# Optimization experiments

Hardware: AMD Instinct MI355X
Metric: run time of the kernel (lower is better)

Reference implementation:

```python
import jax, jax.numpy as jnp
import numpy as np

N, E, F = 32768, 524288, 16          # nodes, edges, num_filters
S_IN, V_IN = 64, 32                  # input irreps: 64x0e + 32x1o  (dim 64 + 96 = 160)
NRBF = 32                            # radial basis size of f_ij
LN2 = float(np.log(2.0))

def ssp(x):
    # shifted softplus, the standard SchNet activation
    return jax.nn.softplus(x) - LN2

def setup_inputs() -> dict:
    key = jax.random.key(0)
    ks = jax.random.split(key, 16)
    x = jax.random.normal(ks[0], (N, S_IN + 3 * V_IN), jnp.float32)
    idx_i = jax.random.randint(ks[1], (E,), 0, N)
    idx_j = jax.random.randint(ks[2], (E,), 0, N)
    f_ij = jax.random.normal(ks[3], (E, NRBF), jnp.float32)
    rcut_ij = jax.random.uniform(ks[4], (E,), jnp.float32)
    Yr_ij = jax.random.normal(ks[5], (E, 4), jnp.float32)  # 1x0e + 1x1o
    # equivariant Linear 1: (64x0e+32x1o) -> num_filters*(1x0e+1x1o) = 16x0e+16x1o
    W1_0e = jax.random.normal(ks[6], (S_IN, F), jnp.float32)
    W1_1o = jax.random.normal(ks[7], (V_IN, F), jnp.float32)
    # filter MLP: NRBF -> F -> num_irreps(6*F)
    mW1 = jax.random.normal(ks[8], (NRBF, F), jnp.float32) / np.sqrt(NRBF)
    mb1 = jnp.zeros((F,), jnp.float32)
    mW2 = jax.random.normal(ks[9], (F, 6 * F), jnp.float32) / np.sqrt(F)
    mb2 = jnp.zeros((6 * F,), jnp.float32)
    # equivariant Linear 2: (2Fx0e+2Fx1o+Fx1e+Fx2e) -> input irreps (1e/2e paths drop)
    W2_0e = jax.random.normal(ks[10], (2 * F, S_IN), jnp.float32)
    W2_1o = jax.random.normal(ks[11], (2 * F, V_IN), jnp.float32)
    # equivariant Linear 3: input irreps -> input irreps
    W3_0e = jax.random.normal(ks[12], (S_IN, S_IN), jnp.float32)
    W3_1o = jax.random.normal(ks[13], (V_IN, V_IN), jnp.float32)
    return dict(x=x, f_ij=f_ij, rcut_ij=rcut_ij, Yr_ij=Yr_ij,
                W1_0e=W1_0e, W1_1o=W1_1o, mW1=mW1, mb1=mb1, mW2=mW2, mb2=mb2,
                W2_0e=W2_0e, W2_1o=W2_1o, W3_0e=W3_0e, W3_1o=W3_1o,
                idx_i=idx_i, idx_j=idx_j)

def reference(x, f_ij, rcut_ij, Yr_ij, W1_0e, W1_1o, mW1, mb1, mW2, mb2,
              W2_0e, W2_1o, W3_0e, W3_1o, idx_i, idx_j):
    n = x.shape[0]
    s = x[:, :S_IN]                                  # [N, 64]  0e channels
    v = x[:, S_IN:].reshape(n, V_IN, 3)              # [N, 32, 3] 1o channels
    # Linear 1 (per-irrep channel mixing, e3nn fan-in normalization)
    s1 = (s @ W1_0e) / np.sqrt(S_IN)                 # [N, F]
    v1 = jnp.einsum('ncd,cf->nfd', v, W1_1o) / np.sqrt(V_IN)  # [N, F, 3]
    # gather neighbor features (x_j = x[idx_j], mul_to_axis -> per-filter irreps)
    sj = s1[idx_j]                                   # [E, F]
    vj = v1[idx_j]                                   # [E, F, 3]
    y0 = Yr_ij[:, 0]                                 # [E]
    y1 = Yr_ij[:, 1:4]                               # [E, 3]
    # tensor product (0e+1o) x (0e+1o) -> 2x0e + 2x1o + 1x1e + 1x2e, per filter
    o0a = sj * y0[:, None]                                            # 0e: 0e x 0e
    o0b = jnp.einsum('efd,ed->ef', vj, y1) / np.sqrt(3.0)             # 0e: 1o.1o
    o1a = sj[:, :, None] * y1[:, None, :]                             # 1o: 0e x 1o
    o1b = vj * y0[:, None, None]                                      # 1o: 1o x 0e
    o1e = jnp.cross(vj, y1[:, None, :]) / np.sqrt(2.0)                # 1e: 1o ^ 1o
    ux, uy, uz = vj[..., 0], vj[..., 1], vj[..., 2]
    wx, wy, wz = y1[:, None, 0], y1[:, None, 1], y1[:, None, 2]
    o2 = jnp.stack([(ux * wy + uy * wx) / np.sqrt(2.0),
                    (uy * wz + uz * wy) / np.sqrt(2.0),
                    (2.0 * uz * wz - ux * wx - uy * wy) / np.sqrt(6.0),
                    (ux * wz + uz * wx) / np.sqrt(2.0),
                    (ux * wx - uy * wy) / np.sqrt(2.0)], axis=-1)      # 2e [E, F, 5]
    # filter MLP on radial features, gated by cutoff; one scalar per irrep
    W = ssp(f_ij @ mW1 + mb1) @ mW2 + mb2            # [E, 6F]
    W = W * rcut_ij[:, None]
    w0a, w0b, w1a, w1b, w1e, w2 = (W[:, k * F:(k + 1) * F] for k in range(6))
    seg = lambda z: jax.ops.segment_sum(z, idx_i, num_segments=N)
    # modulate + scatter-sum into center atoms
    n0a = seg(o0a * w0a); n0b = seg(o0b * w0b)                          # [N, F]
    n1a = seg(o1a * w1a[:, :, None]); n1b = seg(o1b * w1b[:, :, None])  # [N, F, 3]
    n1e = seg(o1e * w1e[:, :, None])                                    # [N, F, 3] (dropped by Linear 2)
    n2 = seg(o2 * w2[:, :, None])                                       # [N, F, 5] (dropped by Linear 2)
    n0 = jnp.concatenate([n0a, n0b], axis=-1)        # [N, 2F] 0e
    n1 = jnp.concatenate([n1a, n1b], axis=1)         # [N, 2F, 3] 1o
    del n1e, n2  # no matching output irrep in input_irreps -> e3nn Linear drops them
    # Linear 2 back to input irreps
    s2 = (n0 @ W2_0e) / np.sqrt(2 * F)               # [N, 64]
    v2 = jnp.einsum('nfd,fc->ncd', n1, W2_1o) / np.sqrt(2 * F)  # [N, 32, 3]
    # scalar activation on l=0 only
    s2 = ssp(s2)
    # Linear 3
    s3 = (s2 @ W3_0e) / np.sqrt(S_IN)
    v3 = jnp.einsum('ncd,ce->ned', v2, W3_1o) / np.sqrt(V_IN)
    return jnp.concatenate([s3, v3.reshape(n, -1)], axis=-1)  # [N, 160]
```

## Files before the change

### kernel.cpp

```cpp
#include <hip/hip_runtime.h>
#include <math.h>

#define NN 32768
#define NE 524288
#define RSTR 32
#define SREC_STR 36

__device__ __forceinline__ float sspf(float x) {
    const float INVLN2 = 1.4426950408889634f;
    const float LN2    = 0.69314718055994530942f;
    float t = __builtin_amdgcn_exp2f(-fabsf(x) * INVLN2);
    return fmaxf(x, 0.0f) + LN2 * __builtin_amdgcn_logf(1.0f + t) - LN2;
}

__global__ __launch_bounds__(256) void hist_kernel(
    const int* __restrict__ idx_i, int* __restrict__ counts, int* __restrict__ rank)
{
    int e = blockIdx.x * 256 + threadIdx.x;
    rank[e] = atomicAdd(&counts[idx_i[e]], 1);
}

__global__ __launch_bounds__(1024) void scan_kernel(
    const int* __restrict__ counts, int* __restrict__ start)
{
    __shared__ int tmp[1024];
    int tid = threadIdx.x;
    int base = tid * 32;
    int local[32];
    int sum = 0;
    const int4* c4 = (const int4*)(counts + base);
#pragma unroll
    for (int q = 0; q < 8; q++) {
        int4 v = c4[q];
        local[q*4+0] = sum; sum += v.x;
        local[q*4+1] = sum; sum += v.y;
        local[q*4+2] = sum; sum += v.z;
        local[q*4+3] = sum; sum += v.w;
    }
    tmp[tid] = sum;
    __syncthreads();
    for (int off = 1; off < 1024; off <<= 1) {
        int v = 0;
        if (tid >= off) v = tmp[tid - off];
        __syncthreads();
        if (tid >= off) tmp[tid] += v;
        __syncthreads();
    }
    int excl = tmp[tid] - sum;
#pragma unroll
    for (int k = 0; k < 32; k++) {
        start[base + k] = excl + local[k];
    }
    if (tid == 1023) start[NN] = tmp[1023];
}

__global__ __launch_bounds__(256) void pack_kernel(
    const float* __restrict__ f_ij,
    const float* __restrict__ rcut_ij,
    const float* __restrict__ Yr,
    const int*   __restrict__ idx_i,
    const int*   __restrict__ idx_j,
    const float* __restrict__ mW1,
    const float* __restrict__ mb1,
    const int*   __restrict__ start,
    const int*   __restrict__ rank,
    float* __restrict__ epack)
{
    __shared__ float sW1[512];
    __shared__ float sb1[16];
    __shared__ float srec[256 * SREC_STR];
    __shared__ int   sslot[256];
    int t = threadIdx.x;
    for (int k = t; k < 512; k += 256) sW1[k] = mW1[k];
    if (t < 16) sb1[t] = mb1[t];
    __syncthreads();

    int e = blockIdx.x * 256 + t;
    float h[16];
#pragma unroll
    for (int f = 0; f < 16; f++) h[f] = sb1[f];
    const float4* frow = (const float4*)(f_ij + (size_t)e * 32);
#pragma unroll
    for (int rq = 0; rq < 8; rq++) {
        float4 fv = frow[rq];
        int r = rq * 4;
#pragma unroll
        for (int f = 0; f < 16; f++)
            h[f] += fv.x * sW1[(r+0)*16+f] + fv.y * sW1[(r+1)*16+f]
                  + fv.z * sW1[(r+2)*16+f] + fv.w * sW1[(r+3)*16+f];
    }
    float rc = rcut_ij[e];
#pragma unroll
    for (int f = 0; f < 16; f++) h[f] = sspf(h[f]) * rc;

    int i = idx_i[e];
    int j = idx_j[e];
    float4 y = ((const float4*)Yr)[e];
    int slot = start[i] + rank[e];

    float* rp = srec + t * SREC_STR;
    float4* rp4 = (float4*)rp;
#pragma unroll
    for (int q = 0; q < 4; q++) rp4[q] = ((float4*)h)[q];
    rp4[4] = y;
    float4 tail; tail.x = rc; tail.y = __int_as_float(j); tail.z = 0.f; tail.w = 0.f;
    rp4[5] = tail;
    float4 z; z.x = 0.f; z.y = 0.f; z.z = 0.f; z.w = 0.f;
    rp4[6] = z;
    rp4[7] = z;
    sslot[t] = slot;
    __syncthreads();

    int lane = t & 63;
    int wbase = t & 192;
    int qi = lane & 7;
#pragma unroll
    for (int g = 0; g < 8; g++) {
        int r = wbase + g * 8 + (lane >> 3);
        int s = sslot[r];
        float4 v = ((const float4*)(srec + r * SREC_STR))[qi];
        ((float4*)(epack + (size_t)s * RSTR))[qi] = v;
    }
}

__global__ __launch_bounds__(256) void embed_kernel(
    const float* __restrict__ x,
    const float* __restrict__ W1s,
    const float* __restrict__ W1v,
    float* __restrict__ embed)
{
    __shared__ float sWs[1024];
    __shared__ float sWv[512];
    int t = threadIdx.x;
    for (int k = t; k < 1024; k += 256) sWs[k] = W1s[k];
    for (int k = t; k < 512;  k += 256) sWv[k] = W1v[k];
    __syncthreads();

    int n = blockIdx.x * 256 + t;
    const float* xr = x + (size_t)n * 160;

    float s1[16];
#pragma unroll
    for (int f = 0; f < 16; f++) s1[f] = 0.f;
#pragma unroll
    for (int cq = 0; cq < 16; cq++) {
        float4 sv = ((const float4*)xr)[cq];
        int c = cq * 4;
#pragma unroll
        for (int f = 0; f < 16; f++) {
            s1[f] += sv.x * sWs[(c+0)*16+f] + sv.y * sWs[(c+1)*16+f]
                   + sv.z * sWs[(c+2)*16+f] + sv.w * sWs[(c+3)*16+f];
        }
    }

    float v1[48];
#pragma unroll
    for (int k = 0; k < 48; k++) v1[k] = 0.f;
#pragma unroll
    for (int q = 0; q < 24; q++) {
        float4 vv = ((const float4*)(xr + 64))[q];
        float vals[4] = {vv.x, vv.y, vv.z, vv.w};
#pragma unroll
        for (int u = 0; u < 4; u++) {
            int m = q * 4 + u;
            int c = m / 3, d = m % 3;
            float val = vals[u];
#pragma unroll
            for (int f = 0; f < 16; f++)
                v1[f*3+d] += val * sWv[c*16+f];
        }
    }

    float ob[64];
    const float is32 = 0.17677669529663688f;
#pragma unroll
    for (int f = 0; f < 16; f++) {
        ob[f]      = s1[f] * 0.125f;
        ob[16 + f] = v1[f*3+0] * is32;
        ob[32 + f] = v1[f*3+1] * is32;
        ob[48 + f] = v1[f*3+2] * is32;
    }

    float4* eo = (float4*)(embed + (size_t)n * 64);
#pragma unroll
    for (int q = 0; q < 16; q++) eo[q] = ((float4*)ob)[q];
}

__global__ __launch_bounds__(256) void nodeagg_kernel(
    const float* __restrict__ embed,
    const float* __restrict__ epack,
    const int*   __restrict__ start,
    const float* __restrict__ mW2,
    const float* __restrict__ mb2,
    float* __restrict__ acc)
{
    __shared__ float sW2[1024];
    int t = threadIdx.x;
    for (int k = t; k < 1024; k += 256)
        sW2[k] = mW2[(k >> 6) * 96 + (k & 63)];
    __syncthreads();

    int gid = blockIdx.x * 256 + t;
    int node = gid >> 4;
    int f = gid & 15;

    float wga[16], wgb[16], wgc[16], wgd[16];
#pragma unroll
    for (int k = 0; k < 16; k++) {
        wga[k] = sW2[k*64 + f];
        wgb[k] = sW2[k*64 + 16 + f];
        wgc[k] = sW2[k*64 + 32 + f];
        wgd[k] = sW2[k*64 + 48 + f];
    }
    float b0a = mb2[f], b0b = mb2[16+f], b1a = mb2[32+f], b1b = mb2[48+f];

    float aa = 0.f, ab = 0.f;
    float A1a0 = 0.f, A1a1 = 0.f, A1a2 = 0.f;
    float A1b0 = 0.f, A1b1 = 0.f, A1b2 = 0.f;

    int s0 = start[node];
    int s1 = start[node+1];

    for (int q = s0; q < s1; q++) {
        const float* rec = epack + (size_t)q * RSTR;
        const float4* r4 = (const float4*)rec;
        float4 h0 = r4[0], h1 = r4[1], h2 = r4[2], h3 = r4[3];
        float4 y  = r4[4];
        float rc  = rec[20];
        int j = __float_as_int(rec[21]);

        const float* em = embed + (size_t)j * 64;
        float sj = em[f];
        float vx = em[16 + f];
        float vy = em[32 + f];
        float vz = em[48 + f];

        float w0a = rc*b0a, w0b = rc*b0b, w1a = rc*b1a, w1b = rc*b1b;
        float h[16] = {h0.x,h0.y,h0.z,h0.w, h1.x,h1.y,h1.z,h1.w,
                       h2.x,h2.y,h2.z,h2.w, h3.x,h3.y,h3.z,h3.w};
#pragma unroll
        for (int k = 0; k < 16; k++) {
            w0a += h[k] * wga[k];
            w0b += h[k] * wgb[k];
            w1a += h[k] * wgc[k];
            w1b += h[k] * wgd[k];
        }

        aa += sj * y.x * w0a;
        ab += (vx*y.y + vy*y.z + vz*y.w) * w0b;
        float sw = sj * w1a;
        A1a0 += sw * y.y;
        A1a1 += sw * y.z;
        A1a2 += sw * y.w;
        float yw = y.x * w1b;
        A1b0 += vx * yw;
        A1b1 += vy * yw;
        A1b2 += vz * yw;
    }

    const float is3 = 0.5773502691896258f;
    float* o = acc + (size_t)node * 128;
    o[f]       = aa;
    o[16 + f]  = ab * is3;
    o[32 + f]  = A1a0;
    o[48 + f]  = A1a1;
    o[64 + f]  = A1a2;
    o[80 + f]  = A1b0;
    o[96 + f]  = A1b1;
    o[112 + f] = A1b2;
}


__device__ __forceinline__ void v2_seg32(const float* a, int d, int cb,
    const float* __restrict__ W2v, float* V2, int ln)
{
    cb = __builtin_amdgcn_readfirstlane(cb);
    const float is32 = 0.17677669529663688f;
    float na[16], nb[16];
    const float4* pa = (const float4*)(a + 32 + 16*d);
    const float4* pb = (const float4*)(a + 80 + 16*d);
#pragma unroll
    for (int q = 0; q < 4; q++) { ((float4*)na)[q] = pa[q]; ((float4*)nb)[q] = pb[q]; }
    float tacc[32];
#pragma unroll
    for (int c = 0; c < 32; c++) tacc[c] = 0.f;
#pragma unroll
    for (int f = 0; f < 16; f++) {
        float fa = na[f], fb = nb[f];
#pragma unroll
        for (int c = 0; c < 32; c++)
            tacc[c] += fa * W2v[f*32 + cb + c] + fb * W2v[(16+f)*32 + cb + c];
    }
    float* row = V2 + (d*64 + ln) * 33 + cb;
#pragma unroll
    for (int c = 0; c < 32; c++) row[c] = tacc[c] * is32;
}

__device__ __forceinline__ void v2_seg16(const float* a, int d, int cb,
    const float* __restrict__ W2v, float* V2, int ln)
{
    cb = __builtin_amdgcn_readfirstlane(cb);
    const float is32 = 0.17677669529663688f;
    float na[16], nb[16];
    const float4* pa = (const float4*)(a + 32 + 16*d);
    const float4* pb = (const float4*)(a + 80 + 16*d);
#pragma unroll
    for (int q = 0; q < 4; q++) { ((float4*)na)[q] = pa[q]; ((float4*)nb)[q] = pb[q]; }
    float tacc[16];
#pragma unroll
    for (int c = 0; c < 16; c++) tacc[c] = 0.f;
#pragma unroll
    for (int f = 0; f < 16; f++) {
        float fa = na[f], fb = nb[f];
#pragma unroll
        for (int c = 0; c < 16; c++)
            tacc[c] += fa * W2v[f*32 + cb + c] + fb * W2v[(16+f)*32 + cb + c];
    }
    float* row = V2 + (d*64 + ln) * 33 + cb;
#pragma unroll
    for (int c = 0; c < 16; c++) row[c] = tacc[c] * is32;
}

__device__ __forceinline__ void v3_seg32(float* o, int d, int cb,
    const float* __restrict__ W3v, const float* V2, int ln)
{
    cb = __builtin_amdgcn_readfirstlane(cb);
    const float is32 = 0.17677669529663688f;
    float tacc[32];
#pragma unroll
    for (int c = 0; c < 32; c++) tacc[c] = 0.f;
    const float* row = V2 + (d*64 + ln) * 33;
#pragma unroll
    for (int k = 0; k < 32; k++) {
        float vk = row[k];
#pragma unroll
        for (int c = 0; c < 32; c++) tacc[c] += vk * W3v[k*32 + cb + c];
    }
#pragma unroll
    for (int c = 0; c < 32; c++) o[64 + (cb+c)*3 + d] = tacc[c] * is32;
}

__device__ __forceinline__ void v3_seg16(float* o, int d, int cb,
    const float* __restrict__ W3v, const float* V2, int ln)
{
    cb = __builtin_amdgcn_readfirstlane(cb);
    const float is32 = 0.17677669529663688f;
    float tacc[16];
#pragma unroll
    for (int c = 0; c < 16; c++) tacc[c] = 0.f;
    const float* row = V2 + (d*64 + ln) * 33;
#pragma unroll
    for (int k = 0; k < 32; k++) {
        float vk = row[k];
#pragma unroll
        for (int c = 0; c < 16; c++) tacc[c] += vk * W3v[k*32 + cb + c];
    }
#pragma unroll
    for (int c = 0; c < 16; c++) o[64 + (cb+c)*3 + d] = tacc[c] * is32;
}

__global__ __launch_bounds__(256) void out_kernel(
    const float* __restrict__ acc,
    const float* __restrict__ W2s,
    const float* __restrict__ W2v,
    const float* __restrict__ W3s,
    const float* __restrict__ W3v,
    float* __restrict__ out)
{
    __shared__ float S2[64*65];
    __shared__ float V2[3*64*33];
    int t = threadIdx.x;
    int w = t >> 6, ln = t & 63;
    int node = blockIdx.x * 64 + ln;
    const float* a = acc + (size_t)node * 128;
    float* o = out + (size_t)node * 160;
    const float is32 = 0.17677669529663688f;

    if (w < 2) {
        int cb = __builtin_amdgcn_readfirstlane(w * 32);
        float n0r[32];
#pragma unroll
        for (int q = 0; q < 8; q++) ((float4*)n0r)[q] = ((const float4*)a)[q];
        float tacc[32];
#pragma unroll
        for (int c = 0; c < 32; c++) tacc[c] = 0.f;
#pragma unroll
        for (int k = 0; k < 32; k++) {
            float nk = n0r[k];
#pragma unroll
            for (int c = 0; c < 32; c++) tacc[c] += nk * W2s[k*64 + cb + c];
        }
        float* row = S2 + ln*65 + cb;
#pragma unroll
        for (int c = 0; c < 32; c++) row[c] = sspf(tacc[c] * is32);
    } else if (w == 2) {
        v2_seg32(a, 0, 0,  W2v, V2, ln);
        v2_seg16(a, 1, 0,  W2v, V2, ln);
    } else {
        v2_seg16(a, 1, 16, W2v, V2, ln);
        v2_seg32(a, 2, 0,  W2v, V2, ln);
    }
    __syncthreads();
    if (w < 2) {
        int cb = __builtin_amdgcn_readfirstlane(w * 32);
        float tacc[32];
#pragma unroll
        for (int c = 0; c < 32; c++) tacc[c] = 0.f;
        const float* row = S2 + ln*65;
#pragma unroll
        for (int k = 0; k < 64; k++) {
            float sk = row[k];
#pragma unroll
            for (int c = 0; c < 32; c++) tacc[c] += sk * W3s[k*64 + cb + c];
        }
#pragma unroll
        for (int q = 0; q < 8; q++) {
            float4 r = {tacc[q*4+0]*0.125f, tacc[q*4+1]*0.125f,
                        tacc[q*4+2]*0.125f, tacc[q*4+3]*0.125f};
            ((float4*)(o + cb))[q] = r;
        }
    } else if (w == 2) {
        v3_seg32(o, 0, 0,  W3v, V2, ln);
        v3_seg16(o, 1, 0,  W3v, V2, ln);
    } else {
        v3_seg16(o, 1, 16, W3v, V2, ln);
        v3_seg32(o, 2, 0,  W3v, V2, ln);
    }
}

extern "C" void kernel_launch(void* const* d_in, const int* in_sizes, int n_in,
                              void* d_out, int out_size, void* d_ws, size_t ws_size,
                              hipStream_t stream) {
    const float* x     = (const float*)d_in[0];
    const float* f_ij  = (const float*)d_in[1];
    const float* rcut  = (const float*)d_in[2];
    const float* Yr    = (const float*)d_in[3];
    const float* W1s   = (const float*)d_in[4];
    const float* W1v   = (const float*)d_in[5];
    const float* mW1   = (const float*)d_in[6];
    const float* mb1   = (const float*)d_in[7];
    const float* mW2   = (const float*)d_in[8];
    const float* mb2   = (const float*)d_in[9];
    const float* W2s   = (const float*)d_in[10];
    const float* W2v   = (const float*)d_in[11];
    const float* W3s   = (const float*)d_in[12];
    const float* W3v   = (const float*)d_in[13];
    const int*   idx_i = (const int*)d_in[14];
    const int*   idx_j = (const int*)d_in[15];
    float* out = (float*)d_out;

    float* fws   = (float*)d_ws;
    float* embed = fws;
    float* acc   = embed + (size_t)NN * 64;
    float* epack = acc   + (size_t)NN * 128;
    int* ibase   = (int*)(epack + (size_t)NE * RSTR);
    int* counts  = ibase;
    int* start   = counts + NN;
    int* rank    = start + NN + 1;

    hipMemsetAsync(counts, 0, (size_t)NN * sizeof(int), stream);
    hist_kernel<<<NE/256, 256, 0, stream>>>(idx_i, counts, rank);
    scan_kernel<<<1, 1024, 0, stream>>>(counts, start);
    pack_kernel<<<NE/256, 256, 0, stream>>>(f_ij, rcut, Yr, idx_i, idx_j,
                                            mW1, mb1, start, rank, epack);
    embed_kernel<<<NN/256, 256, 0, stream>>>(x, W1s, W1v, embed);
    nodeagg_kernel<<<(NN*16)/256, 256, 0, stream>>>(embed, epack, start, mW2, mb2, acc);
    out_kernel<<<NN/64, 256, 0, stream>>>(acc, W2s, W2v, W3s, W3v, out);
}
```

Measured before the change: 338.0 us.

## Spread node aggregation across a full wavefront with interleaved embed layout

The node aggregation kernel now assigns one 64-lane wavefront per node instead of 16 lanes, so each lane computes only one of the four filter weights per edge and accumulates into its own output group. The embed layout is interleaved per filter (s, vx, vy, vz), which lets each lane fetch its neighbor features with a single float4 load. The edge loop is software-pipelined to prefetch the next edge record and neighbor embedding. This cuts per-thread FMA work and register pressure and removes the shared-memory weight staging, but launches four times as many threads and reads each edge record redundantly across the four groups.

```diff
diff --git a/kernel.cpp b/kernel.cpp
--- a/kernel.cpp
+++ b/kernel.cpp
@@ -175,10 +175,10 @@
     const float is32 = 0.17677669529663688f;
 #pragma unroll
     for (int f = 0; f < 16; f++) {
-        ob[f]      = s1[f] * 0.125f;
-        ob[16 + f] = v1[f*3+0] * is32;
-        ob[32 + f] = v1[f*3+1] * is32;
-        ob[48 + f] = v1[f*3+2] * is32;
+        ob[f*4+0] = s1[f] * 0.125f;
+        ob[f*4+1] = v1[f*3+0] * is32;
+        ob[f*4+2] = v1[f*3+1] * is32;
+        ob[f*4+3] = v1[f*3+2] * is32;
     }
 
     float4* eo = (float4*)(embed + (size_t)n * 64);
@@ -194,80 +194,85 @@
     const float* __restrict__ mb2,
     float* __restrict__ acc)
 {
-    __shared__ float sW2[1024];
     int t = threadIdx.x;
-    for (int k = t; k < 1024; k += 256)
-        sW2[k] = mW2[(k >> 6) * 96 + (k & 63)];
-    __syncthreads();
-
-    int gid = blockIdx.x * 256 + t;
-    int node = gid >> 4;
-    int f = gid & 15;
-
-    float wga[16], wgb[16], wgc[16], wgd[16];
-#pragma unroll
-    for (int k = 0; k < 16; k++) {
-        wga[k] = sW2[k*64 + f];
-        wgb[k] = sW2[k*64 + 16 + f];
-        wgc[k] = sW2[k*64 + 32 + f];
-        wgd[k] = sW2[k*64 + 48 + f];
-    }
-    float b0a = mb2[f], b0b = mb2[16+f], b1a = mb2[32+f], b1b = mb2[48+f];
-
-    float aa = 0.f, ab = 0.f;
-    float A1a0 = 0.f, A1a1 = 0.f, A1a2 = 0.f;
-    float A1b0 = 0.f, A1b1 = 0.f, A1b2 = 0.f;
+    int lane = t & 63;
+    int node = (blockIdx.x * 256 + t) >> 6;
+    int grp = lane >> 4;
+    int f = lane & 15;
+
+    float wk[16];
+#pragma unroll
+    for (int k = 0; k < 16; k++) wk[k] = mW2[k * 96 + lane];
+    float bias = mb2[lane];
+
+    bool gs  = (grp == 0) || (grp == 2);
+    bool g1  = (grp == 1);
+    bool g2  = (grp == 2);
+    bool g3  = (grp == 3);
+    bool g23 = (grp >= 2);
+
+    float A0 = 0.f, A1 = 0.f, A2 = 0.f;
 
     int s0 = start[node];
-    int s1 = start[node+1];
-
-    for (int q = s0; q < s1; q++) {
-        const float* rec = epack + (size_t)q * RSTR;
-        const float4* r4 = (const float4*)rec;
+    int s1 = start[node + 1];
+
+    if (s0 < s1) {
+        const float4* r4 = (const float4*)(epack + (size_t)s0 * RSTR);
         float4 h0 = r4[0], h1 = r4[1], h2 = r4[2], h3 = r4[3];
-        float4 y  = r4[4];
-        float rc  = rec[20];
-        int j = __float_as_int(rec[21]);
-
-        const float* em = embed + (size_t)j * 64;
-        float sj = em[f];
-        float vx = em[16 + f];
-        float vy = em[32 + f];
-        float vz = em[48 + f];
-
-        float w0a = rc*b0a, w0b = rc*b0b, w1a = rc*b1a, w1b = rc*b1b;
-        float h[16] = {h0.x,h0.y,h0.z,h0.w, h1.x,h1.y,h1.z,h1.w,
-                       h2.x,h2.y,h2.z,h2.w, h3.x,h3.y,h3.z,h3.w};
-#pragma unroll
-        for (int k = 0; k < 16; k++) {
-            w0a += h[k] * wga[k];
-            w0b += h[k] * wgb[k];
-            w1a += h[k] * wgc[k];
-            w1b += h[k] * wgd[k];
-        }
-
-        aa += sj * y.x * w0a;
-        ab += (vx*y.y + vy*y.z + vz*y.w) * w0b;
-        float sw = sj * w1a;
-        A1a0 += sw * y.y;
-        A1a1 += sw * y.z;
-        A1a2 += sw * y.w;
-        float yw = y.x * w1b;
-        A1b0 += vx * yw;
-        A1b1 += vy * yw;
-        A1b2 += vz * yw;
+        float4 y  = r4[4], tl = r4[5];
+        float4 e4 = ((const float4*)(embed +
+                     (size_t)__float_as_int(tl.y) * 64))[f];
+
+#define NAGG_COMPUTE()                                                      \
+        {                                                                   \
+            float w = tl.x * bias;                                          \
+            w += h0.x*wk[0]  + h0.y*wk[1]  + h0.z*wk[2]  + h0.w*wk[3];      \
+            w += h1.x*wk[4]  + h1.y*wk[5]  + h1.z*wk[6]  + h1.w*wk[7];      \
+            w += h2.x*wk[8]  + h2.y*wk[9]  + h2.z*wk[10] + h2.w*wk[11];     \
+            w += h3.x*wk[12] + h3.y*wk[13] + h3.z*wk[14] + h3.w*wk[15];     \
+            float sj = e4.x, vx = e4.y, vy = e4.z, vz = e4.w;               \
+            float a0 = gs ? sj : vx;                                        \
+            float a1 = g2 ? sj : vy;                                        \
+            float a2 = g2 ? sj : vz;                                        \
+            float c0 = (g1 || g2) ? y.y : y.x;                              \
+            float c1 = g3 ? y.x : y.z;                                      \
+            float c2 = g3 ? y.x : y.w;                                      \
+            float t0 = a0 * c0, t1 = a1 * c1, t2 = a2 * c2;                 \
+            float m0 = g1 ? (t0 + t1 + t2) : t0;                            \
+            float m1 = g23 ? t1 : 0.f;                                      \
+            float m2 = g23 ? t2 : 0.f;                                      \
+            A0 += w * m0;                                                   \
+            A1 += w * m1;                                                   \
+            A2 += w * m2;                                                   \
+        }
+
+        for (int q = s0; q < s1 - 1; q++) {
+            const float4* n4 = (const float4*)(epack + (size_t)(q + 1) * RSTR);
+            float4 nh0 = n4[0], nh1 = n4[1], nh2 = n4[2], nh3 = n4[3];
+            float4 ny  = n4[4], ntl = n4[5];
+
+            NAGG_COMPUTE();
+
+            float4 ne4 = ((const float4*)(embed +
+                          (size_t)__float_as_int(ntl.y) * 64))[f];
+            h0 = nh0; h1 = nh1; h2 = nh2; h3 = nh3;
+            y = ny; tl = ntl; e4 = ne4;
+        }
+        NAGG_COMPUTE();
+#undef NAGG_COMPUTE
     }
 
     const float is3 = 0.5773502691896258f;
     float* o = acc + (size_t)node * 128;
-    o[f]       = aa;
-    o[16 + f]  = ab * is3;
-    o[32 + f]  = A1a0;
-    o[48 + f]  = A1a1;
-    o[64 + f]  = A1a2;
-    o[80 + f]  = A1b0;
-    o[96 + f]  = A1b1;
-    o[112 + f] = A1b2;
+    if (grp == 0) {
+        o[f] = A0;
+    } else if (grp == 1) {
+        o[16 + f] = A0 * is3;
+    } else if (grp == 2) {
+        o[32 + f] = A0; o[48 + f] = A1; o[64 + f] = A2;
+    } else {
+        o[80 + f] = A0; o[96 + f] = A1; o[112 + f] = A2;
+    }
 }
 
 
@@ -464,6 +469,6 @@
     pack_kernel<<<NE/256, 256, 0, stream>>>(f_ij, rcut, Yr, idx_i, idx_j,
                                             mW1, mb1, start, rank, epack);
     embed_kernel<<<NN/256, 256, 0, stream>>>(x, W1s, W1v, embed);
-    nodeagg_kernel<<<(NN*16)/256, 256, 0, stream>>>(embed, epack, start, mW2, mb2, acc);
+    nodeagg_kernel<<<(NN*64)/256, 256, 0, stream>>>(embed, epack, start, mW2, mb2, acc);
     out_kernel<<<NN/64, 256, 0, stream>>>(acc, W2s, W2v, W3s, W3v, out);
 }
```

Result: slower. 462.0 us (+36.7%).

## Sort nodes by degree for load balance and interleave embed layout for vector gathers

Applied to the files above, without the earlier changes.

The scan kernel now also counting-sorts nodes by in-degree, descending, into an order array. The aggregation kernel uses that order, so each wavefront processes nodes of similar degree and loop divergence shrinks. The embed layout is interleaved per filter as (s, vx, vy, vz), so each neighbour gather becomes a single float4 load instead of four scalar loads. The change also drops the shared-memory staging of mW2 in favour of direct loads, adds occupancy hints, and partially rolls the embed loops to cut register pressure. The cost is extra serial work in the single-block scan kernel and a loss of spatial locality in the output writes.

```diff
diff --git a/kernel.cpp b/kernel.cpp
--- a/kernel.cpp
+++ b/kernel.cpp
@@ -21,17 +21,21 @@
 }
 
 __global__ __launch_bounds__(1024) void scan_kernel(
-    const int* __restrict__ counts, int* __restrict__ start)
+    const int* __restrict__ counts, int* __restrict__ start, int* __restrict__ order)
 {
     __shared__ int tmp[1024];
+    __shared__ int bins[64];
+    __shared__ int bcur[64];
     int tid = threadIdx.x;
     int base = tid * 32;
+    int cnt[32];
     int local[32];
     int sum = 0;
     const int4* c4 = (const int4*)(counts + base);
 #pragma unroll
     for (int q = 0; q < 8; q++) {
         int4 v = c4[q];
+        cnt[q*4+0] = v.x; cnt[q*4+1] = v.y; cnt[q*4+2] = v.z; cnt[q*4+3] = v.w;
         local[q*4+0] = sum; sum += v.x;
         local[q*4+1] = sum; sum += v.y;
         local[q*4+2] = sum; sum += v.z;
@@ -52,6 +56,26 @@
         start[base + k] = excl + local[k];
     }
     if (tid == 1023) start[NN] = tmp[1023];
+
+    if (tid < 64) bins[tid] = 0;
+    __syncthreads();
+#pragma unroll
+    for (int k = 0; k < 32; k++) {
+        int d = cnt[k] > 63 ? 63 : cnt[k];
+        atomicAdd(&bins[63 - d], 1);
+    }
+    __syncthreads();
+    if (tid == 0) {
+        int run = 0;
+        for (int b = 0; b < 64; b++) { int c = bins[b]; bcur[b] = run; run += c; }
+    }
+    __syncthreads();
+#pragma unroll
+    for (int k = 0; k < 32; k++) {
+        int d = cnt[k] > 63 ? 63 : cnt[k];
+        int pos = atomicAdd(&bcur[63 - d], 1);
+        order[pos] = base + k;
+    }
 }
 
 __global__ __launch_bounds__(256) void pack_kernel(
@@ -142,32 +166,43 @@
     float s1[16];
 #pragma unroll
     for (int f = 0; f < 16; f++) s1[f] = 0.f;
-#pragma unroll
-    for (int cq = 0; cq < 16; cq++) {
-        float4 sv = ((const float4*)xr)[cq];
-        int c = cq * 4;
-#pragma unroll
-        for (int f = 0; f < 16; f++) {
-            s1[f] += sv.x * sWs[(c+0)*16+f] + sv.y * sWs[(c+1)*16+f]
-                   + sv.z * sWs[(c+2)*16+f] + sv.w * sWs[(c+3)*16+f];
+#pragma unroll 1
+    for (int cc = 0; cc < 4; cc++) {
+        float4 sv[4];
+#pragma unroll
+        for (int q = 0; q < 4; q++) sv[q] = ((const float4*)xr)[cc*4 + q];
+#pragma unroll
+        for (int q = 0; q < 4; q++) {
+            int c = (cc*4 + q) * 4;
+#pragma unroll
+            for (int f = 0; f < 16; f++) {
+                s1[f] += sv[q].x * sWs[(c+0)*16+f] + sv[q].y * sWs[(c+1)*16+f]
+                       + sv[q].z * sWs[(c+2)*16+f] + sv[q].w * sWs[(c+3)*16+f];
+            }
         }
     }
 
     float v1[48];
 #pragma unroll
     for (int k = 0; k < 48; k++) v1[k] = 0.f;
-#pragma unroll
-    for (int q = 0; q < 24; q++) {
-        float4 vv = ((const float4*)(xr + 64))[q];
-        float vals[4] = {vv.x, vv.y, vv.z, vv.w};
-#pragma unroll
-        for (int u = 0; u < 4; u++) {
-            int m = q * 4 + u;
-            int c = m / 3, d = m % 3;
-            float val = vals[u];
-#pragma unroll
-            for (int f = 0; f < 16; f++)
-                v1[f*3+d] += val * sWv[c*16+f];
+#pragma unroll 1
+    for (int cc = 0; cc < 4; cc++) {
+        float4 vv[6];
+#pragma unroll
+        for (int q = 0; q < 6; q++) vv[q] = ((const float4*)(xr + 64))[cc*6 + q];
+#pragma unroll
+        for (int q = 0; q < 6; q++) {
+            float vals[4] = {vv[q].x, vv[q].y, vv[q].z, vv[q].w};
+#pragma unroll
+            for (int u = 0; u < 4; u++) {
+                int ml = q * 4 + u;
+                int c = cc * 8 + ml / 3;
+                int d = ml % 3;
+                float val = vals[u];
+#pragma unroll
+                for (int f = 0; f < 16; f++)
+                    v1[f*3+d] += val * sWv[c*16+f];
+            }
         }
     }
 
@@ -175,10 +210,10 @@
     const float is32 = 0.17677669529663688f;
 #pragma unroll
     for (int f = 0; f < 16; f++) {
-        ob[f]      = s1[f] * 0.125f;
-        ob[16 + f] = v1[f*3+0] * is32;
-        ob[32 + f] = v1[f*3+1] * is32;
-        ob[48 + f] = v1[f*3+2] * is32;
+        ob[f*4+0] = s1[f] * 0.125f;
+        ob[f*4+1] = v1[f*3+0] * is32;
+        ob[f*4+2] = v1[f*3+1] * is32;
+        ob[f*4+3] = v1[f*3+2] * is32;
     }
 
     float4* eo = (float4*)(embed + (size_t)n * 64);
@@ -186,31 +221,27 @@
     for (int q = 0; q < 16; q++) eo[q] = ((float4*)ob)[q];
 }
 
-__global__ __launch_bounds__(256) void nodeagg_kernel(
+__global__ __launch_bounds__(256, 4) void nodeagg_kernel(
     const float* __restrict__ embed,
     const float* __restrict__ epack,
     const int*   __restrict__ start,
+    const int*   __restrict__ order,
     const float* __restrict__ mW2,
     const float* __restrict__ mb2,
     float* __restrict__ acc)
 {
-    __shared__ float sW2[1024];
     int t = threadIdx.x;
-    for (int k = t; k < 1024; k += 256)
-        sW2[k] = mW2[(k >> 6) * 96 + (k & 63)];
-    __syncthreads();
-
     int gid = blockIdx.x * 256 + t;
-    int node = gid >> 4;
+    int node = order[gid >> 4];
     int f = gid & 15;
 
     float wga[16], wgb[16], wgc[16], wgd[16];
 #pragma unroll
     for (int k = 0; k < 16; k++) {
-        wga[k] = sW2[k*64 + f];
-        wgb[k] = sW2[k*64 + 16 + f];
-        wgc[k] = sW2[k*64 + 32 + f];
-        wgd[k] = sW2[k*64 + 48 + f];
+        wga[k] = mW2[k*96 + f];
+        wgb[k] = mW2[k*96 + 16 + f];
+        wgc[k] = mW2[k*96 + 32 + f];
+        wgd[k] = mW2[k*96 + 48 + f];
     }
     float b0a = mb2[f], b0b = mb2[16+f], b1a = mb2[32+f], b1b = mb2[48+f];
 
@@ -222,30 +253,32 @@
     int s1 = start[node+1];
 
     for (int q = s0; q < s1; q++) {
-        const float* rec = epack + (size_t)q * RSTR;
-        const float4* r4 = (const float4*)rec;
+        const float4* r4 = (const float4*)(epack + (size_t)q * RSTR);
         float4 h0 = r4[0], h1 = r4[1], h2 = r4[2], h3 = r4[3];
-        float4 y  = r4[4];
-        float rc  = rec[20];
-        int j = __float_as_int(rec[21]);
-
-        const float* em = embed + (size_t)j * 64;
-        float sj = em[f];
-        float vx = em[16 + f];
-        float vy = em[32 + f];
-        float vz = em[48 + f];
+        float4 y  = r4[4], tl = r4[5];
+        int j = __float_as_int(tl.y);
+        float4 e4 = ((const float4*)(embed + (size_t)j * 64))[f];
+        float rc = tl.x;
 
         float w0a = rc*b0a, w0b = rc*b0b, w1a = rc*b1a, w1b = rc*b1b;
-        float h[16] = {h0.x,h0.y,h0.z,h0.w, h1.x,h1.y,h1.z,h1.w,
-                       h2.x,h2.y,h2.z,h2.w, h3.x,h3.y,h3.z,h3.w};
-#pragma unroll
-        for (int k = 0; k < 16; k++) {
-            w0a += h[k] * wga[k];
-            w0b += h[k] * wgb[k];
-            w1a += h[k] * wgc[k];
-            w1b += h[k] * wgd[k];
-        }
-
+        w0a += h0.x*wga[0]  + h0.y*wga[1]  + h0.z*wga[2]  + h0.w*wga[3]
+             + h1.x*wga[4]  + h1.y*wga[5]  + h1.z*wga[6]  + h1.w*wga[7]
+             + h2.x*wga[8]  + h2.y*wga[9]  + h2.z*wga[10] + h2.w*wga[11]
+             + h3.x*wga[12] + h3.y*wga[13] + h3.z*wga[14] + h3.w*wga[15];
+        w0b += h0.x*wgb[0]  + h0.y*wgb[1]  + h0.z*wgb[2]  + h0.w*wgb[3]
+             + h1.x*wgb[4]  + h1.y*wgb[5]  + h1.z*wgb[6]  + h1.w*wgb[7]
+             + h2.x*wgb[8]  + h2.y*wgb[9]  + h2.z*wgb[10] + h2.w*wgb[11]
+             + h3.x*wgb[12] + h3.y*wgb[13] + h3.z*wgb[14] + h3.w*wgb[15];
+        w1a += h0.x*wgc[0]  + h0.y*wgc[1]  + h0.z*wgc[2]  + h0.w*wgc[3]
+             + h1.x*wgc[4]  + h1.y*wgc[5]  + h1.z*wgc[6]  + h1.w*wgc[7]
+             + h2.x*wgc[8]  + h2.y*wgc[9]  + h2.z*wgc[10] + h2.w*wgc[11]
+             + h3.x*wgc[12] + h3.y*wgc[13] + h3.z*wgc[14] + h3.w*wgc[15];
+        w1b += h0.x*wgd[0]  + h0.y*wgd[1]  + h0.z*wgd[2]  + h0.w*wgd[3]
+             + h1.x*wgd[4]  + h1.y*wgd[5]  + h1.z*wgd[6]  + h1.w*wgd[7]
+             + h2.x*wgd[8]  + h2.y*wgd[9]  + h2.z*wgd[10] + h2.w*wgd[11]
+             + h3.x*wgd[12] + h3.y*wgd[13] + h3.z*wgd[14] + h3.w*wgd[15];
+
+        float sj = e4.x, vx = e4.y, vy = e4.z, vz = e4.w;
         aa += sj * y.x * w0a;
         ab += (vx*y.y + vy*y.z + vz*y.w) * w0b;
         float sw = sj * w1a;
@@ -457,13 +490,15 @@
     int* counts  = ibase;
     int* start   = counts + NN;
     int* rank    = start + NN + 1;
+    int* order   = rank + NE;
 
     hipMemsetAsync(counts, 0, (size_t)NN * sizeof(int), stream);
     hist_kernel<<<NE/256, 256, 0, stream>>>(idx_i, counts, rank);
-    scan_kernel<<<1, 1024, 0, stream>>>(counts, start);
+    scan_kernel<<<1, 1024, 0, stream>>>(counts, start, order);
     pack_kernel<<<NE/256, 256, 0, stream>>>(f_ij, rcut, Yr, idx_i, idx_j,
                                             mW1, mb1, start, rank, epack);
     embed_kernel<<<NN/256, 256, 0, stream>>>(x, W1s, W1v, embed);
-    nodeagg_kernel<<<(NN*16)/256, 256, 0, stream>>>(embed, epack, start, mW2, mb2, acc);
+    nodeagg_kernel<<<(NN*16)/256, 256, 0, stream>>>(embed, epack, start, order,
+                                                    mW2, mb2, acc);
     out_kernel<<<NN/64, 256, 0, stream>>>(acc, W2s, W2v, W3s, W3v, out);
 }
```

Result: no change. 333.7 us (-1.3%).
